# Kernel optimization log

Hardware: AMD Instinct MI355X
Metric: run time of the kernel (lower is better)

The kernel has to match this reference:

```python
import jax, jax.numpy as jnp
import numpy as np

SPATIAL = 8  # spatial_size


def setup_inputs() -> dict:
    key = jax.random.key(0)
    k1, k2 = jax.random.split(key)
    B, C, T, H, W = 8, 1, 16, 500, 500
    inp = jax.random.normal(k1, (B, C, T, H, W), dtype=jnp.float32)
    stdv = 1.0 / np.sqrt(T)  # matches reset_parameters scaling
    weight = jax.random.uniform(k2, (T, 4, 4), dtype=jnp.float32, minval=-stdv, maxval=stdv)
    return {"input": inp, "weight": weight, "pad_h": 512, "pad_w": 512,
            "n_patch_h": 127, "n_patch_w": 127}


def reference(input, weight, pad_h, pad_w, n_patch_h, n_patch_w):
    B, C, T, H, W = input.shape
    step = weight.shape[1]  # spatial_size // 2 (overlapping)
    s = SPATIAL

    # zero-pad bottom/right to the padded frame size
    x = jnp.pad(input, ((0, 0), (0, 0), (0, 0), (0, pad_h - H), (0, pad_w - W)))

    # weight.repeat(B, C, 1, n_patch_h+1, n_patch_w+1): tile step-blocks over frame;
    # broadcast over (B, C) instead of materializing the full repeat.
    w_tiled = jnp.tile(weight, (1, n_patch_h + 1, n_patch_w + 1))  # (T, pad_h, pad_w)

    # masked multiply + temporal sum -> coded snapshot (B, C, pad_h, pad_w)
    output = jnp.einsum('bcthw,thw->bchw', x, w_tiled)

    # overlapping patch extraction: unfold(2, s, step).unfold(3, s, step)
    hh = (jnp.arange(n_patch_h) * step)[:, None] + jnp.arange(s)  # (nph, s)
    ww = (jnp.arange(n_patch_w) * step)[:, None] + jnp.arange(s)  # (npw, s)
    patches = output[:, :, hh[:, None, :, None], ww[None, :, None, :]]  # (B,C,nph,npw,s,s)

    # permute(0,1,2,3,5,4) then flatten to (B, C*nph*npw, s*s)
    patches = jnp.swapaxes(patches, -1, -2)
    patches = patches.reshape(B, -1, s * s)

    return patches, output[:, :, :H, :W]
```

## Files before the change

kernel.cpp:

```cpp
#include <hip/hip_runtime.h>

#define B_DIM 8
#define T_DIM 16
#define H_IN 500
#define W_IN 500
#define NPH 127
#define NPW 127
#define LSTR 516
#define NT 512
#define BANDS 32
#define ROWS 16

typedef float f4 __attribute__((ext_vector_type(4)));

__global__ __launch_bounds__(NT) void k_band(const float* __restrict__ in,
                                             const float* __restrict__ wgt,
                                             float* __restrict__ patches,
                                             float* __restrict__ crop) {
    __shared__ float lds[ROWS * LSTR];
    __shared__ f4 wlds[T_DIM * 4];
    int tid = threadIdx.x;
    if (tid < T_DIM * 4) wlds[tid] = reinterpret_cast<const f4*>(wgt)[tid];

    int orig = blockIdx.x;
    int b = orig & 7;
    int q = orig >> 3;
    __syncthreads();

    #pragma unroll
    for (int k = 0; k < 4; ++k) {
        int e = tid + k * NT;
        int r = e >> 7;
        int c = (e & 127) * 4;
        int h = q * ROWS + r;
        f4 acc = {0.f, 0.f, 0.f, 0.f};
        if (h < H_IN && c < W_IN) {
            const float* base = in + (size_t)b * T_DIM * (H_IN * W_IN) + h * W_IN + c;
            int hr = h & 3;
            f4 xv[T_DIM];
            #pragma unroll
            for (int t = 0; t < T_DIM; ++t)
                xv[t] = *reinterpret_cast<const f4*>(base + (size_t)t * (H_IN * W_IN));
            #pragma unroll
            for (int t = 0; t < T_DIM; ++t)
                acc += xv[t] * wlds[t * 4 + hr];
            *reinterpret_cast<f4*>(crop + ((size_t)b * H_IN + h) * W_IN + c) = acc;
        }
        *reinterpret_cast<f4*>(&lds[r * LSTR + c]) = acc;
    }
    __syncthreads();

    f4* pbase = reinterpret_cast<f4*>(patches)
              + ((size_t)b * NPH + (size_t)4 * q) * NPW * 16;
    #pragma unroll
    for (int sub = 0; sub < 3; ++sub) {
        f4* dst = pbase + (size_t)sub * NPW * 16;
        for (int e4 = tid; e4 < NPW * 16; e4 += NT) {
            int i0 = (e4 & 1) * 4;
            int j  = (e4 >> 1) & 7;
            int pw = e4 >> 4;
            int col = pw * 4 + j;
            int r0 = sub * 4 + i0;
            f4 v;
            v.x = lds[(r0 + 0) * LSTR + col];
            v.y = lds[(r0 + 1) * LSTR + col];
            v.z = lds[(r0 + 2) * LSTR + col];
            v.w = lds[(r0 + 3) * LSTR + col];
            dst[e4] = v;
        }
    }
    if (q < BANDS - 1) {
        f4* dst = pbase + (size_t)3 * NPW * 16;
        for (int e = tid; e < NPW * 8; e += NT) {
            int j  = e & 7;
            int pw = e >> 3;
            int col = pw * 4 + j;
            f4 v;
            v.x = lds[12 * LSTR + col];
            v.y = lds[13 * LSTR + col];
            v.z = lds[14 * LSTR + col];
            v.w = lds[15 * LSTR + col];
            dst[pw * 16 + j * 2] = v;
        }
    }
    if (q > 0) {
        f4* dst = reinterpret_cast<f4*>(patches)
                + ((size_t)b * NPH + (size_t)(4 * q - 1)) * NPW * 16;
        for (int e = tid; e < NPW * 8; e += NT) {
            int j  = e & 7;
            int pw = e >> 3;
            int col = pw * 4 + j;
            f4 v;
            v.x = lds[0 * LSTR + col];
            v.y = lds[1 * LSTR + col];
            v.z = lds[2 * LSTR + col];
            v.w = lds[3 * LSTR + col];
            dst[pw * 16 + j * 2 + 1] = v;
        }
    }
}

extern "C" void kernel_launch(void* const* d_in, const int* in_sizes, int n_in,
                              void* d_out, int out_size, void* d_ws, size_t ws_size,
                              hipStream_t stream) {
    const float* in  = (const float*)d_in[0];
    const float* wgt = (const float*)d_in[1];
    float* out     = (float*)d_out;
    float* patches = out;
    float* crop    = out + (size_t)B_DIM * NPH * NPW * 64;

    k_band<<<B_DIM * BANDS, NT, 0, stream>>>(in, wgt, patches, crop);
}
```

Measured before the change: 30.39 us.

## Interleave band input loads with patch emission via double-buffered registers

Restructures the band kernel so row groups are loaded into two register buffers and processed in stages. Patch emission from LDS for already-computed rows overlaps with global loads for later rows, with syncs between stages. This aims to hide load latency behind patch stores instead of serializing all loads before all emission. The cost is more synchronisation points and higher register pressure from holding two 16-element f4 buffers, which may reduce occupancy.

```diff
diff --git a/kernel.cpp b/kernel.cpp
--- a/kernel.cpp
+++ b/kernel.cpp
@@ -4,6 +4,7 @@
 #define T_DIM 16
 #define H_IN 500
 #define W_IN 500
+#define HW (H_IN * W_IN)
 #define NPH 127
 #define NPW 127
 #define LSTR 516
@@ -27,33 +28,38 @@
     int q = orig >> 3;
     __syncthreads();
 
-    #pragma unroll
-    for (int k = 0; k < 4; ++k) {
-        int e = tid + k * NT;
-        int r = e >> 7;
-        int c = (e & 127) * 4;
+    int rc = tid >> 7;
+    int c  = (tid & 127) * 4;
+    bool cv = (c < W_IN);
+    const float* ibase = in + (size_t)b * T_DIM * HW + c;
+
+    f4 xA[T_DIM], xB[T_DIM];
+
+    auto issue = [&](int k, f4* xv) {
+        int h = q * ROWS + k * 4 + rc;
+        if (h < H_IN && cv) {
+            const float* p = ibase + h * W_IN;
+            #pragma unroll
+            for (int t = 0; t < T_DIM; ++t)
+                xv[t] = *reinterpret_cast<const f4*>(p + (size_t)t * HW);
+        }
+    };
+    auto fma_store = [&](int k, f4* xv) {
+        int r = k * 4 + rc;
         int h = q * ROWS + r;
         f4 acc = {0.f, 0.f, 0.f, 0.f};
-        if (h < H_IN && c < W_IN) {
-            const float* base = in + (size_t)b * T_DIM * (H_IN * W_IN) + h * W_IN + c;
+        if (h < H_IN && cv) {
             int hr = h & 3;
-            f4 xv[T_DIM];
-            #pragma unroll
-            for (int t = 0; t < T_DIM; ++t)
-                xv[t] = *reinterpret_cast<const f4*>(base + (size_t)t * (H_IN * W_IN));
             #pragma unroll
             for (int t = 0; t < T_DIM; ++t)
                 acc += xv[t] * wlds[t * 4 + hr];
             *reinterpret_cast<f4*>(crop + ((size_t)b * H_IN + h) * W_IN + c) = acc;
         }
         *reinterpret_cast<f4*>(&lds[r * LSTR + c]) = acc;
-    }
-    __syncthreads();
-
+    };
     f4* pbase = reinterpret_cast<f4*>(patches)
               + ((size_t)b * NPH + (size_t)4 * q) * NPW * 16;
-    #pragma unroll
-    for (int sub = 0; sub < 3; ++sub) {
+    auto emit_full = [&](int sub) {
         f4* dst = pbase + (size_t)sub * NPW * 16;
         for (int e4 = tid; e4 < NPW * 16; e4 += NT) {
             int i0 = (e4 & 1) * 4;
@@ -68,21 +74,16 @@
             v.w = lds[(r0 + 3) * LSTR + col];
             dst[e4] = v;
         }
-    }
-    if (q < BANDS - 1) {
-        f4* dst = pbase + (size_t)3 * NPW * 16;
-        for (int e = tid; e < NPW * 8; e += NT) {
-            int j  = e & 7;
-            int pw = e >> 3;
-            int col = pw * 4 + j;
-            f4 v;
-            v.x = lds[12 * LSTR + col];
-            v.y = lds[13 * LSTR + col];
-            v.z = lds[14 * LSTR + col];
-            v.w = lds[15 * LSTR + col];
-            dst[pw * 16 + j * 2] = v;
-        }
-    }
+    };
+
+    issue(0, xA);
+    issue(1, xB);
+    fma_store(0, xA);
+    fma_store(1, xB);
+    __syncthreads();
+
+    issue(2, xA);
+    emit_full(0);
     if (q > 0) {
         f4* dst = reinterpret_cast<f4*>(patches)
                 + ((size_t)b * NPH + (size_t)(4 * q - 1)) * NPW * 16;
@@ -98,6 +99,29 @@
             dst[pw * 16 + j * 2 + 1] = v;
         }
     }
+    fma_store(2, xA);
+    __syncthreads();
+
+    issue(3, xB);
+    emit_full(1);
+    fma_store(3, xB);
+    __syncthreads();
+
+    emit_full(2);
+    if (q < BANDS - 1) {
+        f4* dst = pbase + (size_t)3 * NPW * 16;
+        for (int e = tid; e < NPW * 8; e += NT) {
+            int j  = e & 7;
+            int pw = e >> 3;
+            int col = pw * 4 + j;
+            f4 v;
+            v.x = lds[12 * LSTR + col];
+            v.y = lds[13 * LSTR + col];
+            v.z = lds[14 * LSTR + col];
+            v.w = lds[15 * LSTR + col];
+            dst[pw * 16 + j * 2] = v;
+        }
+    }
 }
 
 extern "C" void kernel_launch(void* const* d_in, const int* in_sizes, int n_in,
```

Result: slower. 31.55 us (+3.8%).
